# Kernel optimization log

Hardware: AMD Instinct MI355X
Metric: run time of the kernel (lower is better)

Reference implementation:

```python
import jax, jax.numpy as jnp
import numpy as np

B, N, M, H = 2, 1024, 1024, 128
SCALE = 1.0 / (float(H) ** 0.4)  # scale_factor = 1/hidden_size**0.4


def setup_inputs() -> dict:
    key = jax.random.key(0)
    k1, k2, k3, k4, k5 = jax.random.split(key, 5)
    return {
        "queries": jax.random.normal(k1, (B, N, H), dtype=jnp.float32),
        "keys": jax.random.normal(k2, (B, M, H), dtype=jnp.float32),
        "values": jax.random.normal(k3, (B, N, 1, 1), dtype=jnp.float32),
        "W": jax.random.normal(k4, (H, H), dtype=jnp.float32) * (1.0 / np.sqrt(H)),
        "b": jax.random.normal(k5, (H,), dtype=jnp.float32) * 0.01,
    }


def reference(queries, keys, values, W, b):
    # shared projection for queries and keys (dropout disabled: eval-mode reference)
    qp = jnp.einsum("bnh,oh->bno", queries, W) + b  # [B,N,H]
    kp = jnp.einsum("bmh,oh->bmo", keys, W) + b     # [B,M,H]
    # sum over H of (qp[n] + kp[m]) == qp.sum(-1)[n] + kp.sum(-1)[m]
    qs = qp.sum(-1)  # [B,N]
    ks = kp.sum(-1)  # [B,M]
    logits = SCALE * (qs[:, :, None] + ks[:, None, :])  # [B,N,M]
    w = jax.nn.softmax(logits, axis=-1)                 # [B,N,M]
    # matmul([B,N,M,1], values[B,N,1,1]).squeeze(-1) == w * v scalar per (b,n)
    out = w * values[:, :, 0, 0][:, :, None]            # [B,N,M]
    return out
```

## Files before the change

kernel.cpp:

```cpp
#include <hip/hip_runtime.h>
#include <hip/hip_bf16.h>

#define B_ 2
#define N_ 1024
#define M_ 1024
#define H_ 128
#define SCALE_F 0.14358729f

__global__ void __launch_bounds__(1024) softmax_p_kernel(
    const float* __restrict__ keys,
    const float* __restrict__ W,
    float* __restrict__ p)
{
    const int b = blockIdx.x;
    const int m = threadIdx.x;
    __shared__ float wpart[8][H_];
    __shared__ float wsum[H_];
    __shared__ float red[16];
    __shared__ float bc[2];

    {
        const int col = m & (H_ - 1);
        const int grp = m >> 7;
        float s = 0.f;
        #pragma unroll
        for (int i = 0; i < 16; ++i)
            s += W[(grp * 16 + i) * H_ + col];
        wpart[grp][col] = s;
    }
    __syncthreads();
    if (m < H_) {
        float t = 0.f;
        #pragma unroll
        for (int g = 0; g < 8; ++g) t += wpart[g][m];
        wsum[m] = t;
    }
    __syncthreads();

    const float4* krow = (const float4*)(keys + ((size_t)b * M_ + m) * H_);
    const float4* w4   = (const float4*)wsum;
    float acc = 0.f;
    #pragma unroll
    for (int i = 0; i < H_ / 4; ++i) {
        float4 k4 = krow[i];
        float4 ww = w4[i];
        acc = fmaf(k4.x, ww.x, acc);
        acc = fmaf(k4.y, ww.y, acc);
        acc = fmaf(k4.z, ww.z, acc);
        acc = fmaf(k4.w, ww.w, acc);
    }
    const float logit = SCALE_F * acc;

    const int lane = m & 63;
    const int wid  = m >> 6;

    float v = logit;
    #pragma unroll
    for (int off = 32; off > 0; off >>= 1) v = fmaxf(v, __shfl_down(v, off));
    if (lane == 0) red[wid] = v;
    __syncthreads();
    if (wid == 0) {
        float t = (lane < 16) ? red[lane] : -3.4e38f;
        #pragma unroll
        for (int off = 8; off > 0; off >>= 1) t = fmaxf(t, __shfl_down(t, off));
        if (lane == 0) bc[0] = t;
    }
    __syncthreads();
    const float gmax = bc[0];
    const float e = __expf(logit - gmax);
    __syncthreads();

    v = e;
    #pragma unroll
    for (int off = 32; off > 0; off >>= 1) v += __shfl_down(v, off);
    if (lane == 0) red[wid] = v;
    __syncthreads();
    if (wid == 0) {
        float t = (lane < 16) ? red[lane] : 0.f;
        #pragma unroll
        for (int off = 8; off > 0; off >>= 1) t += __shfl_down(t, off);
        if (lane == 0) bc[1] = 1.0f / t;
    }
    __syncthreads();

    p[b * M_ + m] = e * bc[1];
}

__global__ void __launch_bounds__(256) outer_write_kernel(
    const float* __restrict__ p,
    const float* __restrict__ values,
    float4* __restrict__ out)
{
    const int j  = blockIdx.x * blockDim.x + threadIdx.x;
    const int m4 = j & (M_ / 4 - 1);
    const int n  = (j >> 8) & (N_ - 1);
    const int b  = j >> 18;

    const float4 pv = ((const float4*)p)[(b << 8) + m4];
    const float  v  = values[(b << 10) + n];
    float4 o;
    o.x = pv.x * v; o.y = pv.y * v; o.z = pv.z * v; o.w = pv.w * v;
    out[j] = o;
}

extern "C" void kernel_launch(void* const* d_in, const int* in_sizes, int n_in,
                              void* d_out, int out_size, void* d_ws, size_t ws_size,
                              hipStream_t stream) {
    const float* keys   = (const float*)d_in[1];
    const float* values = (const float*)d_in[2];
    const float* W      = (const float*)d_in[3];
    float* out = (float*)d_out;
    float* p   = (float*)d_ws;

    softmax_p_kernel<<<B_, 1024, 0, stream>>>(keys, W, p);

    const int total4 = B_ * N_ * M_ / 4;
    outer_write_kernel<<<total4 / 256, 256, 0, stream>>>(p, values, (float4*)out);
}
```

Measured before the change: 85.50 us.

## Fuse softmax and outer-product write into one kernel with redundant per-block softmax

Merges the two kernels into one launch of 256 blocks. Each block recomputes the W column sums, the key logits and the softmax for its batch, keeps the probabilities in LDS, and writes 8 output rows. This removes the second launch, the workspace round-trip and the serial dependency on a 2-block kernel, at the cost of redundant projection and softmax work in every block (128x more key reads, mostly cache hits).

```diff
diff --git a/kernel.cpp b/kernel.cpp
--- a/kernel.cpp
+++ b/kernel.cpp
@@ -1,5 +1,4 @@
 #include <hip/hip_runtime.h>
-#include <hip/hip_bf16.h>
 
 #define B_ 2
 #define N_ 1024
@@ -7,15 +6,20 @@
 #define H_ 128
 #define SCALE_F 0.14358729f
 
-__global__ void __launch_bounds__(1024) softmax_p_kernel(
+__global__ void __launch_bounds__(1024) fused_kernel(
     const float* __restrict__ keys,
+    const float* __restrict__ values,
     const float* __restrict__ W,
-    float* __restrict__ p)
+    float4* __restrict__ out)
 {
-    const int b = blockIdx.x;
-    const int m = threadIdx.x;
+    const int blk   = blockIdx.x;
+    const int b     = blk >> 7;
+    const int nbase = (blk & 127) << 3;
+    const int m     = threadIdx.x;
+
     __shared__ float wpart[8][H_];
     __shared__ float wsum[H_];
+    __shared__ float p_lds[M_];
     __shared__ float red[16];
     __shared__ float bc[2];
 
@@ -68,7 +72,7 @@
     __syncthreads();
     const float gmax = bc[0];
     const float e = __expf(logit - gmax);
-    __syncthreads();
+    p_lds[m] = e;
 
     v = e;
     #pragma unroll
@@ -82,25 +86,20 @@
         if (lane == 0) bc[1] = 1.0f / t;
     }
     __syncthreads();
+    const float inv = bc[1];
 
-    p[b * M_ + m] = e * bc[1];
-}
-
-__global__ void __launch_bounds__(256) outer_write_kernel(
-    const float* __restrict__ p,
-    const float* __restrict__ values,
-    float4* __restrict__ out)
-{
-    const int j  = blockIdx.x * blockDim.x + threadIdx.x;
-    const int m4 = j & (M_ / 4 - 1);
-    const int n  = (j >> 8) & (N_ - 1);
-    const int b  = j >> 18;
-
-    const float4 pv = ((const float4*)p)[(b << 8) + m4];
-    const float  v  = values[(b << 10) + n];
-    float4 o;
-    o.x = pv.x * v; o.y = pv.y * v; o.z = pv.z * v; o.w = pv.w * v;
-    out[j] = o;
+    const float4* p4 = (const float4*)p_lds;
+    const int m4 = m & 255;
+    const int rr = m >> 8;
+    #pragma unroll
+    for (int pass = 0; pass < 2; ++pass) {
+        const int n  = nbase + pass * 4 + rr;
+        const float vv = values[(b << 10) + n] * inv;
+        const float4 pv = p4[m4];
+        float4 o;
+        o.x = pv.x * vv; o.y = pv.y * vv; o.z = pv.z * vv; o.w = pv.w * vv;
+        out[(((size_t)(b << 10) + n) << 8) + m4] = o;
+    }
 }
 
 extern "C" void kernel_launch(void* const* d_in, const int* in_sizes, int n_in,
@@ -109,11 +108,7 @@
     const float* keys   = (const float*)d_in[1];
     const float* values = (const float*)d_in[2];
     const float* W      = (const float*)d_in[3];
-    float* out = (float*)d_out;
-    float* p   = (float*)d_ws;
+    float4* out = (float4*)d_out;
 
-    softmax_p_kernel<<<B_, 1024, 0, stream>>>(keys, W, p);
-
-    const int total4 = B_ * N_ * M_ / 4;
-    outer_write_kernel<<<total4 / 256, 256, 0, stream>>>(p, values, (float4*)out);
+    fused_kernel<<<256, 1024, 0, stream>>>(keys, values, W, out);
 }
```

Result: faster. 83.60 us (-2.2%).
